# Kernel tuning notes

Measured on AMD Instinct MI355X. Metric: run time of the kernel, lower is better.

Reference implementation:

```python
import jax, jax.numpy as jnp
from jax import lax
import numpy as np

EPS_DENOM = 1e-5
EPS_NCC = 1e-5
HIGH = 0.5  # IntensityNormalization(high=0.5): min-max rescale of weights to [0, high]


def _box_conv(v, kernel):
    # Dense ones-kernel 3D box filter, VALID padding, stride 1 (NCDHW / OIDHW).
    return lax.conv_general_dilated(
        v, kernel, window_strides=(1, 1, 1), padding='VALID',
        dimension_numbers=('NCDHW', 'OIDHW', 'NCDHW'))


def setup_inputs() -> dict:
    key = jax.random.key(0)
    k1, k2 = jax.random.split(key)
    shape = (2, 1, 160, 192, 160)
    y_pred = jax.random.normal(k1, shape, dtype=jnp.float32)
    y_true = jax.random.normal(k2, shape, dtype=jnp.float32)
    kernel = jnp.ones((1, 1, 7, 7, 7), dtype=jnp.float32)
    return {"y_pred": y_pred, "y_true": y_true, "kernel": kernel}


def reference(y_pred, y_true, kernel):
    nw = kernel.sum()  # = 343 for a 7^3 ones kernel
    x, y = y_pred, y_true
    sum_x = _box_conv(x, kernel)
    sum_y = _box_conv(y, kernel)
    sum_x2 = _box_conv(x * x, kernel)
    sum_y2 = _box_conv(y * y, kernel)
    sum_xy = _box_conv(x * y, kernel)

    mean_x = sum_x / nw
    mean_y = sum_y / nw
    num = sum_xy + mean_x * mean_y * nw - mean_x * sum_y - mean_y * sum_x
    denom_0 = mean_x * mean_x * nw + sum_x2 - 2.0 * mean_x * sum_x
    denom_1 = mean_y * mean_y * nw + sum_y2 - 2.0 * mean_y * sum_y
    denom = denom_0 * denom_1

    valid = denom > EPS_DENOM
    safe_denom = jnp.where(valid, denom, 1.0)
    ncc = jnp.where(valid, num / jnp.sqrt(safe_denom), 0.0)
    invalid = (ncc < -1.0 - EPS_NCC) | (ncc > 1.0 + EPS_NCC)
    ncc = jnp.where(invalid, 0.0, ncc)
    all_valid = valid & ~invalid

    # Intensity normalization of weights: min-max rescale of local variance sum
    # over the valid voxels to [0, HIGH], then normalize to sum to 1.
    v = 0.5 * (denom_0 + denom_1)
    vmin = jnp.min(jnp.where(all_valid, v, jnp.inf))
    vmax = jnp.max(jnp.where(all_valid, v, -jnp.inf))
    w = jnp.where(all_valid, (v - vmin) / (vmax - vmin + 1e-12) * HIGH, 0.0)
    w = w / w.sum()

    return 1.0 - jnp.sum(jnp.where(all_valid, ncc, 0.0) * w)
```

## Files before the change

### kernel.cpp

```cpp
#include <hip/hip_runtime.h>
#include <math.h>

#define NN 2
#define DD 160
#define HH 192
#define WW 160
#define DO 154
#define HO 186
#define WO 154

#define NWO 3
#define NHO 47
#define ZCH 8
#define ZOC 20
#define NB (NWO * NHO * NN * ZCH)

#define LDS_SYNC() do { __builtin_amdgcn_s_waitcnt(0xC07F); __builtin_amdgcn_s_barrier(); } while (0)

__device__ __forceinline__ float block_sum(float v, float* sm) {
  int tid = threadIdx.x;
  sm[tid] = v;
  __syncthreads();
#pragma unroll
  for (int off = 128; off > 0; off >>= 1) {
    if (tid < off) sm[tid] += sm[tid + off];
    __syncthreads();
  }
  float r = sm[0];
  __syncthreads();
  return r;
}

__device__ __forceinline__ float block_min(float v, float* sm) {
  int tid = threadIdx.x;
  sm[tid] = v;
  __syncthreads();
#pragma unroll
  for (int off = 128; off > 0; off >>= 1) {
    if (tid < off) sm[tid] = fminf(sm[tid], sm[tid + off]);
    __syncthreads();
  }
  float r = sm[0];
  __syncthreads();
  return r;
}

__global__ __launch_bounds__(256, 4) void ncc_fused(const float* __restrict__ X,
                                                    const float* __restrict__ Y,
                                                    float* __restrict__ part) {
  __shared__ __align__(16) float R[5][10][64];
  __shared__ __align__(16) float Mh[5][4][64];
  __shared__ float sm[256];

  const int tid = threadIdx.x;
  const int tx = tid & 63, ty = tid >> 6;
  const int wo0 = blockIdx.x * 64;
  const int ho0 = blockIdx.y * 4;
  const int n   = blockIdx.z >> 3;
  const int ck  = blockIdx.z & 7;
  const int z0  = ck * ZOC;
  const int zout = min(ZOC, DO - z0);
  const int nslice = zout + 6;

  const int wo = wo0 + tx, ho = ho0 + ty;
  const bool act = (wo < WO) && (ho < HO);

  const size_t slice = (size_t)HH * WW;
  const float* Xn = X + (size_t)n * DD * slice;
  const float* Yn = Y + (size_t)n * DD * slice;
  const float inv_nw = 1.0f / 343.0f;
  const float LO = -1.0f - 1e-5f, HI = 1.0f + 1e-5f;

  const int pA  = tid;
  const bool hasA = (pA < 160);
  const int rA  = pA >> 4;
  const int cqA = (pA & 15) << 2;
  const int hA  = ho0 + rA;
  const int baseW = wo0 + cqA;
  const bool okA  = hasA && (hA < HH) && (baseW < WO);
  const bool tail = okA && (baseW + 9 >= WW);
  const float* XrowA = Xn + (size_t)hA * WW + baseW;
  const float* YrowA = Yn + (size_t)hA * WW + baseW;

  float4 lx0 = {0,0,0,0}, lx1 = {0,0,0,0}, ly0 = {0,0,0,0}, ly1 = {0,0,0,0};
  float2 lx2 = {0,0}, ly2 = {0,0};

  auto loadA = [&](int s_in) {
    if (okA) {
      const float* xp = XrowA + (size_t)(z0 + s_in) * slice;
      const float* yp = YrowA + (size_t)(z0 + s_in) * slice;
      lx0 = *(const float4*)xp; lx1 = *(const float4*)(xp + 4);
      ly0 = *(const float4*)yp; ly1 = *(const float4*)(yp + 4);
      if (!tail) { lx2 = *(const float2*)(xp + 8); ly2 = *(const float2*)(yp + 8); }
      else       { lx2 = make_float2(0.f, 0.f);    ly2 = make_float2(0.f, 0.f); }
    }
  };

  auto storeA = [&]() {
    if (okA) {
      float x0=lx0.x,x1=lx0.y,x2=lx0.z,x3=lx0.w,x4=lx1.x,x5=lx1.y,x6=lx1.z,x7=lx1.w,x8=lx2.x,x9=lx2.y;
      float y0=ly0.x,y1=ly0.y,y2=ly0.z,y3=ly0.w,y4=ly1.x,y5=ly1.y,y6=ly1.z,y7=ly1.w,y8=ly2.x,y9=ly2.y;
      {
        float a = x0+x1+x2+x3+x4+x5+x6;
        float b = a - x0 + x7, c = b - x1 + x8, d = c - x2 + x9;
        *(float4*)&R[0][rA][cqA] = make_float4(a, b, c, d);
      }
      {
        float a = y0+y1+y2+y3+y4+y5+y6;
        float b = a - y0 + y7, c = b - y1 + y8, d = c - y2 + y9;
        *(float4*)&R[1][rA][cqA] = make_float4(a, b, c, d);
      }
      {
        float a = x0*x0+x1*x1+x2*x2+x3*x3+x4*x4+x5*x5+x6*x6;
        float b = a - x0*x0 + x7*x7, c = b - x1*x1 + x8*x8, d = c - x2*x2 + x9*x9;
        *(float4*)&R[2][rA][cqA] = make_float4(a, b, c, d);
      }
      {
        float a = y0*y0+y1*y1+y2*y2+y3*y3+y4*y4+y5*y5+y6*y6;
        float b = a - y0*y0 + y7*y7, c = b - y1*y1 + y8*y8, d = c - y2*y2 + y9*y9;
        *(float4*)&R[3][rA][cqA] = make_float4(a, b, c, d);
      }
      {
        float a = x0*y0+x1*y1+x2*y2+x3*y3+x4*y4+x5*y5+x6*y6;
        float b = a - x0*y0 + x7*y7, c = b - x1*y1 + x8*y8, d = c - x2*y2 + x9*y9;
        *(float4*)&R[4][rA][cqA] = make_float4(a, b, c, d);
      }
    }
  };

  auto phaseH = [&]() {
    {
      const int ch = ty, w = tx;
      const float* rp = &R[ch][0][w];
      float r0=rp[0],r1=rp[64],r2=rp[128],r3=rp[192],r4=rp[256],
            r5=rp[320],r6=rp[384],r7=rp[448],r8=rp[512],r9=rp[576];
      float m0 = r0+r1+r2+r3+r4+r5+r6;
      float m1 = m0 - r0 + r7, m2 = m1 - r1 + r8, m3 = m2 - r2 + r9;
      Mh[ch][0][w]=m0; Mh[ch][1][w]=m1; Mh[ch][2][w]=m2; Mh[ch][3][w]=m3;
    }
    if (tx < 16) {
      const int w = ty * 16 + tx;
      const float* rp = &R[4][0][w];
      float r0=rp[0],r1=rp[64],r2=rp[128],r3=rp[192],r4=rp[256],
            r5=rp[320],r6=rp[384],r7=rp[448],r8=rp[512],r9=rp[576];
      float m0 = r0+r1+r2+r3+r4+r5+r6;
      float m1 = m0 - r0 + r7, m2 = m1 - r1 + r8, m3 = m2 - r2 + r9;
      Mh[4][0][w]=m0; Mh[4][1][w]=m1; Mh[4][2][w]=m2; Mh[4][3][w]=m3;
    }
  };

  float a0[7], a1[7], a2[7], a3[7], a4[7];
#pragma unroll
  for (int j = 0; j < 7; ++j) { a0[j]=0.f; a1[j]=0.f; a2[j]=0.f; a3[j]=0.f; a4[j]=0.f; }
  float p_snv = 0.f, p_sn = 0.f, p_sv = 0.f, p_cnt = 0.f, p_vmin = 3.4e38f;

  loadA(0);
  storeA();
  __syncthreads();

  for (int sb = 0; sb < nslice; sb += 7) {
#pragma unroll
    for (int u = 0; u < 7; ++u) {
      const int s = sb + u;
      if (s < nslice) {
        if (s + 1 < nslice) loadA(s + 1);
        phaseH();
        LDS_SYNC();
        {
          float m0 = Mh[0][ty][tx], m1 = Mh[1][ty][tx], m2 = Mh[2][ty][tx],
                m3 = Mh[3][ty][tx], m4 = Mh[4][ty][tx];
#pragma unroll
          for (int j = 0; j < 7; ++j) {
            a0[j]+=m0; a1[j]+=m1; a2[j]+=m2; a3[j]+=m3; a4[j]+=m4;
          }
          if (s >= 6 && act) {
            float zs0=a0[u], zs1=a1[u], zs2=a2[u], zs3=a3[u], zs4=a4[u];
            float num = zs4 - zs0 * zs1 * inv_nw;
            float d0  = zs2 - zs0 * zs0 * inv_nw;
            float d1  = zs3 - zs1 * zs1 * inv_nw;
            float den = d0 * d1;
            if (den > 1e-5f) {
              float ncc = num * __frsqrt_rn(den);
              if (ncc >= LO && ncc <= HI) {
                float v = 0.5f * (d0 + d1);
                p_snv += ncc * v; p_sn += ncc; p_sv += v; p_cnt += 1.f;
                p_vmin = fminf(p_vmin, v);
              }
            }
          }
          a0[u]=0.f; a1[u]=0.f; a2[u]=0.f; a3[u]=0.f; a4[u]=0.f;
        }
        if (s + 1 < nslice) storeA();
        LDS_SYNC();
      }
    }
  }

  float bsnv = block_sum(p_snv, sm);
  float bsn  = block_sum(p_sn, sm);
  float bsv  = block_sum(p_sv, sm);
  float bcnt = block_sum(p_cnt, sm);
  float bmin = block_min(p_vmin, sm);
  if (tid == 0) {
    const int bid = blockIdx.x + NWO * (blockIdx.y + NHO * blockIdx.z);
    float* pp = part + (size_t)bid * 8;
    pp[0] = bsnv; pp[1] = bsn; pp[2] = bsv; pp[3] = bcnt; pp[4] = bmin;
  }
}

__global__ __launch_bounds__(256) void fin(const float* __restrict__ part,
                                           float* __restrict__ out) {
  __shared__ float sm[256];
  const int tid = threadIdx.x;
  float s0 = 0.f, s1 = 0.f, s2 = 0.f, s3 = 0.f, vm = 3.4e38f;
  for (int b = tid; b < NB; b += 256) {
    const float* pp = part + (size_t)b * 8;
    s0 += pp[0]; s1 += pp[1]; s2 += pp[2]; s3 += pp[3];
    vm = fminf(vm, pp[4]);
  }
  s0 = block_sum(s0, sm);
  s1 = block_sum(s1, sm);
  s2 = block_sum(s2, sm);
  s3 = block_sum(s3, sm);
  vm = block_min(vm, sm);
  if (tid == 0) {
    out[0] = 1.0f - (s0 - vm * s1) / (s2 - vm * s3);
  }
}

extern "C" void kernel_launch(void* const* d_in, const int* in_sizes, int n_in,
                              void* d_out, int out_size, void* d_ws, size_t ws_size,
                              hipStream_t stream) {
  const float* X = (const float*)d_in[0];
  const float* Y = (const float*)d_in[1];

  float* part = (float*)d_ws;

  dim3 g(NWO, NHO, NN * ZCH);
  ncc_fused<<<g, 256, 0, stream>>>(X, Y, part);
  fin<<<1, 256, 0, stream>>>(part, (float*)d_out);
}
```

Before: 177.4 us.

## Replace finalize kernel with atomic last-block reduction and raise occupancy hint

Drops the separate finalize kernel. Each block now atomically adds its partial sums into a workspace accumulator and folds its minimum in through an order-preserving unsigned encoding, and the last block to finish computes the output. This removes one kernel launch and the partials round trip, but adds three small memset operations and atomic contention across 2256 blocks. The launch bound is raised from 4 to 6 blocks per CU, and the extra R[4] row-sum work moves to the last wavefront.

```diff
diff --git a/kernel.cpp b/kernel.cpp
--- a/kernel.cpp
+++ b/kernel.cpp
@@ -17,6 +17,11 @@
 
 #define LDS_SYNC() do { __builtin_amdgcn_s_waitcnt(0xC07F); __builtin_amdgcn_s_barrier(); } while (0)
 
+__device__ __forceinline__ unsigned mono_f2u(float f) {
+  unsigned u = __float_as_uint(f);
+  return (u & 0x80000000u) ? ~u : (u | 0x80000000u);
+}
+
 __device__ __forceinline__ float block_sum(float v, float* sm) {
   int tid = threadIdx.x;
   sm[tid] = v;
@@ -45,9 +50,10 @@
   return r;
 }
 
-__global__ __launch_bounds__(256, 4) void ncc_fused(const float* __restrict__ X,
+__global__ __launch_bounds__(256, 6) void ncc_fused(const float* __restrict__ X,
                                                     const float* __restrict__ Y,
-                                                    float* __restrict__ part) {
+                                                    float* __restrict__ acc,
+                                                    float* __restrict__ out) {
   __shared__ __align__(16) float R[5][10][64];
   __shared__ __align__(16) float Mh[5][4][64];
   __shared__ float sm[256];
@@ -138,8 +144,8 @@
       float m1 = m0 - r0 + r7, m2 = m1 - r1 + r8, m3 = m2 - r2 + r9;
       Mh[ch][0][w]=m0; Mh[ch][1][w]=m1; Mh[ch][2][w]=m2; Mh[ch][3][w]=m3;
     }
-    if (tx < 16) {
-      const int w = ty * 16 + tx;
+    if (tid >= 192) {
+      const int w = tid - 192;
       const float* rp = &R[4][0][w];
       float r0=rp[0],r1=rp[64],r2=rp[128],r3=rp[192],r4=rp[256],
             r5=rp[320],r6=rp[384],r7=rp[448],r8=rp[512],r9=rp[576];
@@ -202,29 +208,23 @@
   float bcnt = block_sum(p_cnt, sm);
   float bmin = block_min(p_vmin, sm);
   if (tid == 0) {
-    const int bid = blockIdx.x + NWO * (blockIdx.y + NHO * blockIdx.z);
-    float* pp = part + (size_t)bid * 8;
-    pp[0] = bsnv; pp[1] = bsn; pp[2] = bsv; pp[3] = bcnt; pp[4] = bmin;
-  }
-}
-
-__global__ __launch_bounds__(256) void fin(const float* __restrict__ part,
-                                           float* __restrict__ out) {
-  __shared__ float sm[256];
-  const int tid = threadIdx.x;
-  float s0 = 0.f, s1 = 0.f, s2 = 0.f, s3 = 0.f, vm = 3.4e38f;
-  for (int b = tid; b < NB; b += 256) {
-    const float* pp = part + (size_t)b * 8;
-    s0 += pp[0]; s1 += pp[1]; s2 += pp[2]; s3 += pp[3];
-    vm = fminf(vm, pp[4]);
-  }
-  s0 = block_sum(s0, sm);
-  s1 = block_sum(s1, sm);
-  s2 = block_sum(s2, sm);
-  s3 = block_sum(s3, sm);
-  vm = block_min(vm, sm);
-  if (tid == 0) {
-    out[0] = 1.0f - (s0 - vm * s1) / (s2 - vm * s3);
+    atomicAdd(&acc[0], bsnv);
+    atomicAdd(&acc[1], bsn);
+    atomicAdd(&acc[2], bsv);
+    atomicAdd(&acc[3], bcnt);
+    atomicMin((unsigned*)acc + 4, mono_f2u(bmin));
+    __threadfence();
+    unsigned prev = atomicAdd((unsigned*)acc + 5, 1u);
+    if (prev == NB - 1) {
+      float snv = atomicAdd(&acc[0], 0.f);
+      float sn  = atomicAdd(&acc[1], 0.f);
+      float sv  = atomicAdd(&acc[2], 0.f);
+      float cnt = atomicAdd(&acc[3], 0.f);
+      unsigned um = atomicMin((unsigned*)acc + 4, 0xFFFFFFFFu);
+      unsigned bits = (um & 0x80000000u) ? (um ^ 0x80000000u) : ~um;
+      float vmin = __uint_as_float(bits);
+      out[0] = 1.0f - (snv - vmin * sn) / (sv - vmin * cnt);
+    }
   }
 }
 
@@ -234,9 +234,11 @@
   const float* X = (const float*)d_in[0];
   const float* Y = (const float*)d_in[1];
 
-  float* part = (float*)d_ws;
+  float* acc = (float*)d_ws;
+  hipMemsetAsync(acc, 0, 16, stream);
+  hipMemsetAsync((char*)acc + 16, 0xFF, 4, stream);
+  hipMemsetAsync((char*)acc + 20, 0, 4, stream);
 
   dim3 g(NWO, NHO, NN * ZCH);
-  ncc_fused<<<g, 256, 0, stream>>>(X, Y, part);
-  fin<<<1, 256, 0, stream>>>(part, (float*)d_out);
-}
+  ncc_fused<<<g, 256, 0, stream>>>(X, Y, acc, (float*)d_out);
+}
```

After: 330.9 us. +86.5%, slower.
